# Optimization experiments

Hardware: AMD Instinct MI355X
Metric: run time of the kernel (lower is better)

## Reference

```python
import jax, jax.numpy as jnp
import numpy as np

B, L, C, O, K, KN, A = 32, 4096, 256, 256, 3, 4, 16
BN_EPS = 1e-5


def setup_inputs() -> dict:
    key = jax.random.key(0)
    ks = jax.random.split(key, 12)
    x = jax.random.normal(ks[0], (B, L, C), dtype=jnp.float32)
    # ODConv weight bank [kernel_num, out, in//groups, k], kaiming-ish scale
    weight = jax.random.normal(ks[1], (KN, O, C, K), dtype=jnp.float32) * np.sqrt(2.0 / (O * K))
    w_fc = jax.random.normal(ks[2], (A, C), dtype=jnp.float32) * np.sqrt(2.0 / A)
    bn_gamma = jnp.ones((A,), jnp.float32)
    bn_beta = jnp.zeros((A,), jnp.float32)
    bn_mean = jnp.zeros((A,), jnp.float32)
    bn_var = jnp.ones((A,), jnp.float32)
    w_ch = jax.random.normal(ks[3], (C, A), dtype=jnp.float32) * np.sqrt(2.0 / C)
    b_ch = jnp.zeros((C,), jnp.float32)
    w_fil = jax.random.normal(ks[4], (O, A), dtype=jnp.float32) * np.sqrt(2.0 / O)
    b_fil = jnp.zeros((O,), jnp.float32)
    w_sp = jax.random.normal(ks[5], (K, A), dtype=jnp.float32) * np.sqrt(2.0 / K)
    b_sp = jnp.zeros((K,), jnp.float32)
    w_ker = jax.random.normal(ks[6], (KN, A), dtype=jnp.float32) * np.sqrt(2.0 / KN)
    b_ker = jnp.zeros((KN,), jnp.float32)
    return {"x": x, "weight": weight, "w_fc": w_fc, "bn_gamma": bn_gamma,
            "bn_beta": bn_beta, "bn_mean": bn_mean, "bn_var": bn_var,
            "w_ch": w_ch, "b_ch": b_ch, "w_fil": w_fil, "b_fil": b_fil,
            "w_sp": w_sp, "b_sp": b_sp, "w_ker": w_ker, "b_ker": b_ker}


def reference(x, weight, w_fc, bn_gamma, bn_beta, bn_mean, bn_var,
              w_ch, b_ch, w_fil, b_fil, w_sp, b_sp, w_ker, b_ker):
    # x: [B, L, C] channels-last; attention head uses global-avg-pooled features
    pooled = x.mean(axis=1)                                   # [B, C]
    h = pooled @ w_fc.T                                       # [B, A] (1x1 conv, no bias)
    h = (h - bn_mean) * jax.lax.rsqrt(bn_var + BN_EPS) * bn_gamma + bn_beta
    h = jax.nn.relu(h)
    # temperature = 1.0
    ch_att = jax.nn.sigmoid(h @ w_ch.T + b_ch)                # [B, C]  channel attention
    fil_att = jax.nn.sigmoid(h @ w_fil.T + b_fil)             # [B, O]  filter attention
    sp_att = jax.nn.sigmoid(h @ w_sp.T + b_sp)                # [B, K]  spatial attention
    ker_att = jax.nn.softmax(h @ w_ker.T + b_ker, axis=1)     # [B, KN] kernel attention
    # aggregate per-sample dynamic kernel: [B, O, C, K]
    agg_w = jnp.einsum('bk,bn,noik->boik', sp_att, ker_att, weight)
    xs = x.transpose(0, 2, 1) * ch_att[:, :, None]            # [B, C, L]

    def conv1(xi, wi):  # xi: [C, L], wi: [O, C, K]
        return jax.lax.conv_general_dilated(
            xi[None], wi, window_strides=(1,), padding=[(1, 1)],
            rhs_dilation=(1,), dimension_numbers=('NCH', 'OIH', 'NCH'))[0]

    out = jax.vmap(conv1)(xs, agg_w)                          # [B, O, L]
    return out * fil_att[:, :, None]
```

## Files before the change

kernel.cpp:

```cpp
#include <hip/hip_runtime.h>
#include <hip/hip_bf16.h>
#include <stdint.h>

#define B_ 32
#define L_ 4096
#define C_ 256
#define O_ 256
#define K_ 3
#define KN_ 4
#define A_ 16

typedef unsigned short u16;
typedef __attribute__((ext_vector_type(8))) short bf16x8;
typedef __attribute__((ext_vector_type(4))) float f32x4;

static __device__ __forceinline__ u16 f2bf(float f) {
    union { float f; uint32_t u; } v; v.f = f;
    uint32_t u = v.u;
    u += 0x7fffu + ((u >> 16) & 1u);
    return (u16)(u >> 16);
}

__global__ __launch_bounds__(256) void pool_partial_k(const float* __restrict__ x,
                                                      float* __restrict__ part) {
    int bid = blockIdx.x;
    int b = bid >> 5, ch = bid & 31;
    int c = threadIdx.x;
    const float* p = x + (size_t)(b * L_ + ch * 128) * C_ + c;
    float s = 0.f;
    #pragma unroll 4
    for (int l = 0; l < 128; ++l) s += p[(size_t)l * C_];
    part[((size_t)bid << 8) + c] = s;
}

__global__ __launch_bounds__(256) void att_k(const float* __restrict__ part,
    const float* __restrict__ w_fc, const float* __restrict__ bn_g,
    const float* __restrict__ bn_b, const float* __restrict__ bn_m,
    const float* __restrict__ bn_v,
    const float* __restrict__ w_ch, const float* __restrict__ b_ch,
    const float* __restrict__ w_fil, const float* __restrict__ b_fil,
    const float* __restrict__ w_sp, const float* __restrict__ b_sp,
    const float* __restrict__ w_ker, const float* __restrict__ b_ker,
    float* __restrict__ ch_att, float* __restrict__ fil_att,
    float* __restrict__ sp_att, float* __restrict__ ker_att) {
    __shared__ float pooled[C_];
    __shared__ float h[A_];
    int b = blockIdx.x, t = threadIdx.x;
    float s = 0.f;
    for (int j = 0; j < 32; ++j) s += part[(((size_t)(b * 32 + j)) << 8) + t];
    pooled[t] = s * (1.0f / L_);
    __syncthreads();
    if (t < A_) {
        float acc = 0.f;
        for (int c = 0; c < C_; ++c) acc += pooled[c] * w_fc[t * C_ + c];
        float sc = bn_g[t] * rsqrtf(bn_v[t] + 1e-5f);
        acc = (acc - bn_m[t]) * sc + bn_b[t];
        h[t] = fmaxf(acc, 0.f);
    }
    __syncthreads();
    {
        float a1 = b_ch[t], a2 = b_fil[t];
        for (int a = 0; a < A_; ++a) { a1 += h[a] * w_ch[t * A_ + a]; a2 += h[a] * w_fil[t * A_ + a]; }
        ch_att[b * C_ + t]  = 1.f / (1.f + expf(-a1));
        fil_att[b * O_ + t] = 1.f / (1.f + expf(-a2));
    }
    if (t < K_) {
        float acc = b_sp[t];
        for (int a = 0; a < A_; ++a) acc += h[a] * w_sp[t * A_ + a];
        sp_att[b * 4 + t] = 1.f / (1.f + expf(-acc));
    }
    if (t == 0) {
        float lg[KN_], m = -1e30f;
        for (int n = 0; n < KN_; ++n) {
            float acc = b_ker[n];
            for (int a = 0; a < A_; ++a) acc += h[a] * w_ker[n * A_ + a];
            lg[n] = acc; m = fmaxf(m, acc);
        }
        float ss = 0.f;
        for (int n = 0; n < KN_; ++n) { lg[n] = expf(lg[n] - m); ss += lg[n]; }
        for (int n = 0; n < KN_; ++n) ker_att[b * 4 + n] = lg[n] / ss;
    }
}

__global__ __launch_bounds__(256) void wfrag_k(const float* __restrict__ weight,
    const float* __restrict__ ch_att, const float* __restrict__ fil_att,
    const float* __restrict__ sp_att, const float* __restrict__ ker_att,
    u16* __restrict__ wf) {
    __shared__ float wlds[64 * 97];
    int beta = blockIdx.x;
    int ob = beta & 15, ic = (beta >> 4) & 7, bg = beta >> 7;
    int t = threadIdx.x;

    const size_t blk_base = (size_t)(ob * 16) * 768 + ic * 96;
    #pragma unroll
    for (int j = 0; j < 24; ++j) {
        int ei = t + (j << 8);
        int r = ei / 96, c = ei - r * 96;
        int n = r >> 4, ol = r & 15;
        wlds[r * 97 + c] = weight[((size_t)n * 256 + ol) * 768 + blk_base + c];
    }
    __syncthreads();

    int lane = t & 63, q = t >> 6;
    int o_l = lane & 15, ig = lane >> 4;
    int i0 = ig << 3;
    int o = (ob << 4) + o_l;
    int ig0 = (ic << 5) + i0;

    float wl[4][3][8];
    #pragma unroll
    for (int n = 0; n < 4; ++n) {
        int rb = (n * 16 + o_l) * 97;
        #pragma unroll
        for (int e = 0; e < 8; ++e) {
            int cb = rb + (i0 + e) * 3;
            wl[n][0][e] = wlds[cb];
            wl[n][1][e] = wlds[cb + 1];
            wl[n][2][e] = wlds[cb + 2];
        }
    }

    #pragma unroll
    for (int bi = 0; bi < 2; ++bi) {
        int b = (bg << 3) + (q << 1) + bi;
        float ka0 = ker_att[b * 4 + 0], ka1 = ker_att[b * 4 + 1];
        float ka2 = ker_att[b * 4 + 2], ka3 = ker_att[b * 4 + 3];
        float fil = fil_att[b * O_ + o];
        float ch8[8];
        *reinterpret_cast<float4*>(ch8)     = *reinterpret_cast<const float4*>(ch_att + b * C_ + ig0);
        *reinterpret_cast<float4*>(ch8 + 4) = *reinterpret_cast<const float4*>(ch_att + b * C_ + ig0 + 4);
        #pragma unroll
        for (int tap = 0; tap < 3; ++tap) {
            float fs = fil * sp_att[b * 4 + tap];
            union { u16 h[8]; uint4 v; } pk;
            #pragma unroll
            for (int e = 0; e < 8; ++e) {
                float acc = ka0 * wl[0][tap][e] + ka1 * wl[1][tap][e]
                          + ka2 * wl[2][tap][e] + ka3 * wl[3][tap][e];
                pk.h[e] = f2bf(acc * fs * ch8[e]);
            }
            size_t idx = ((((size_t)(b * 24 + tap * 8 + ic) * 16 + ob) * 64) + lane) << 3;
            *reinterpret_cast<uint4*>(wf + idx) = pk.v;
        }
    }
}

__global__ __launch_bounds__(512, 4) void conv_k(const float* __restrict__ x,
    const u16* __restrict__ wf, float* __restrict__ out) {
    __shared__ uint4 lds4[4160];
    char* lp = (char*)lds4;
    int phys = blockIdx.x;
    int logical = ((phys & 7) << 7) + (phys >> 3);
    int b = logical >> 5, lb = logical & 31;
    int l0 = lb << 7;
    int tid = threadIdx.x;
    const size_t xbase = (size_t)b * L_ * C_;

    #pragma unroll 4
    for (int it = 0; it < 17; ++it) {
        int id = tid + (it << 9);
        if (id < 8320) {
            int r  = id >> 6;
            int i  = (id & 63) << 2;
            int lg = l0 - 1 + r;
            float4 v = make_float4(0.f, 0.f, 0.f, 0.f);
            if (lg >= 0 && lg < L_)
                v = *reinterpret_cast<const float4*>(x + xbase + (size_t)lg * C_ + i);
            ushort4 hv;
            hv.x = f2bf(v.x); hv.y = f2bf(v.y); hv.z = f2bf(v.z); hv.w = f2bf(v.w);
            int slot = (i >> 3) ^ (r & 7);
            int off = r * 512 + slot * 16 + ((i >> 2) & 1) * 8;
            *reinterpret_cast<ushort4*>(lp + off) = hv;
        }
    }
    __syncthreads();

    int w = tid >> 6, lane = tid & 63;
    int wr = w & 3, wc = w >> 2;
    int lrow = lane & 15;
    int g = lane >> 4;

    f32x4 acc[4][4] = {};

    for (int kc = 0; kc < 24; ++kc) {
        int t  = kc >> 3;
        int ic = kc & 7;
        bf16x8 af[4], bfr[4];
        const u16* wp = wf + ((((size_t)(b * 24 + kc) * 16 + wr * 4) * 64 + lane) << 3);
        #pragma unroll
        for (int m = 0; m < 4; ++m)
            af[m] = *reinterpret_cast<const bf16x8*>(wp + (m << 9));
        int slotbase = (ic << 2) + g;
        #pragma unroll
        for (int n = 0; n < 4; ++n) {
            int row = wc * 64 + n * 16 + lrow + t;
            int off = row * 512 + ((slotbase ^ (row & 7)) << 4);
            bfr[n] = *reinterpret_cast<const bf16x8*>(lp + off);
        }
        #pragma unroll
        for (int m = 0; m < 4; ++m)
            #pragma unroll
            for (int n = 0; n < 4; ++n)
                acc[m][n] = __builtin_amdgcn_mfma_f32_16x16x32_bf16(af[m], bfr[n], acc[m][n], 0, 0, 0);
    }

    __syncthreads();

    float* ep = (float*)(lp + w * 8192);
    size_t obase = (size_t)b * O_ * L_;
    int lcol = l0 + wc * 64;
    #pragma unroll
    for (int c2 = 0; c2 < 2; ++c2) {
        #pragma unroll
        for (int m2 = 0; m2 < 2; ++m2) {
            int m = c2 * 2 + m2;
            #pragma unroll
            for (int n = 0; n < 4; ++n) {
                int l_loc = n * 16 + lrow;
                int sl = (l_loc >> 2);
                #pragma unroll
                for (int j = 0; j < 4; ++j) {
                    int o_loc = m2 * 16 + g * 4 + j;
                    ep[o_loc * 64 + ((sl ^ o_loc) & 15) * 4 + (l_loc & 3)] = acc[m][n][j];
                }
            }
        }
        #pragma unroll
        for (int og = 0; og < 8; ++og) {
            int o_loc = og * 4 + g;
            int l4 = lrow;
            float4 v = *reinterpret_cast<float4*>(ep + o_loc * 64 + ((l4 ^ o_loc) & 15) * 4);
            int o = wr * 64 + c2 * 32 + o_loc;
            *reinterpret_cast<float4*>(out + obase + (size_t)o * L_ + lcol + l4 * 4) = v;
        }
        if (c2 == 0) __syncthreads();
    }
}

extern "C" void kernel_launch(void* const* d_in, const int* in_sizes, int n_in,
                              void* d_out, int out_size, void* d_ws, size_t ws_size,
                              hipStream_t stream) {
    const float* x      = (const float*)d_in[0];
    const float* weight = (const float*)d_in[1];
    const float* w_fc   = (const float*)d_in[2];
    const float* bn_g   = (const float*)d_in[3];
    const float* bn_b   = (const float*)d_in[4];
    const float* bn_m   = (const float*)d_in[5];
    const float* bn_v   = (const float*)d_in[6];
    const float* w_ch   = (const float*)d_in[7];
    const float* b_ch   = (const float*)d_in[8];
    const float* w_fil  = (const float*)d_in[9];
    const float* b_fil  = (const float*)d_in[10];
    const float* w_sp   = (const float*)d_in[11];
    const float* b_sp   = (const float*)d_in[12];
    const float* w_ker  = (const float*)d_in[13];
    const float* b_ker  = (const float*)d_in[14];
    float* out = (float*)d_out;
    char*  ws  = (char*)d_ws;

    float* part    = (float*)ws;
    float* ch_att  = (float*)(ws + (1 << 20));
    float* fil_att = ch_att + 32 * 256;
    float* sp_att  = fil_att + 32 * 256;
    float* ker_att = sp_att + 32 * 4;
    u16*   wfrag   = (u16*)(ws + (1 << 20) + 70 * 1024);

    pool_partial_k<<<1024, 256, 0, stream>>>(x, part);
    att_k<<<32, 256, 0, stream>>>(part, w_fc, bn_g, bn_b, bn_m, bn_v,
                                  w_ch, b_ch, w_fil, b_fil, w_sp, b_sp, w_ker, b_ker,
                                  ch_att, fil_att, sp_att, ker_att);
    wfrag_k<<<512, 256, 0, stream>>>(weight, ch_att, fil_att, sp_att, ker_att, wfrag);
    conv_k<<<1024, 512, 0, stream>>>(x, wfrag, out);
}
```

Baseline: 107.5 us.

## Fuse bf16 conversion of x into pooling pass and stage via direct LDS loads

New measurement: 120.4 us. 12.0% more time.

```diff
diff --git a/kernel.cpp b/kernel.cpp
--- a/kernel.cpp
+++ b/kernel.cpp
@@ -9,16 +9,56 @@
 #define K_ 3
 #define KN_ 4
 #define A_ 16
+#define LP_ 4098
 
 typedef unsigned short u16;
 typedef __attribute__((ext_vector_type(8))) short bf16x8;
 typedef __attribute__((ext_vector_type(4))) float f32x4;
+
+#define GLDS16(gp, lp_) __builtin_amdgcn_global_load_lds( \
+    (const __attribute__((address_space(1))) void*)(gp),  \
+    (__attribute__((address_space(3))) void*)(lp_), 16, 0, 0)
 
 static __device__ __forceinline__ u16 f2bf(float f) {
     union { float f; uint32_t u; } v; v.f = f;
     uint32_t u = v.u;
     u += 0x7fffu + ((u >> 16) & 1u);
     return (u16)(u >> 16);
+}
+
+__global__ __launch_bounds__(256) void poolcvt_k(const float* __restrict__ x,
+                                                 u16* __restrict__ xb,
+                                                 float* __restrict__ part) {
+    __shared__ float red[4][256];
+    int bid = blockIdx.x;
+    int b = bid >> 5, chunk = bid & 31;
+    int t = threadIdx.x;
+    int w = t >> 6, lane = t & 63;
+    int c0 = lane << 2;
+    int h = lane >> 5;
+    int grp = (lane & 31) >> 1;
+    int sub = lane & 1;
+    f32x4 s = {0.f, 0.f, 0.f, 0.f};
+    const float* xp = x + ((size_t)b * L_ + (size_t)chunk * 128) * C_ + c0;
+    u16* xbb = xb + ((size_t)b * LP_ + (size_t)chunk * 128 + 1) * 256;
+    #pragma unroll 4
+    for (int it = 0; it < 32; ++it) {
+        int rl = it * 4 + w;
+        int l = chunk * 128 + rl;
+        float4 v = *reinterpret_cast<const float4*>(xp + (size_t)rl * C_);
+        s.x += v.x; s.y += v.y; s.z += v.z; s.w += v.w;
+        ushort4 hv;
+        hv.x = f2bf(v.x); hv.y = f2bf(v.y); hv.z = f2bf(v.z); hv.w = f2bf(v.w);
+        int slot = grp ^ ((l + 1) & 7);
+        *reinterpret_cast<ushort4*>(xbb + (size_t)rl * 256 + h * 128 + slot * 8 + sub * 4) = hv;
+    }
+    *reinterpret_cast<f32x4*>(&red[w][c0]) = s;
+    __syncthreads();
+    part[((size_t)bid << 8) + t] = red[0][t] + red[1][t] + red[2][t] + red[3][t];
+    if (chunk == 0 && t < 64)
+        *reinterpret_cast<ushort4*>(xb + (size_t)b * LP_ * 256 + t * 4) = make_ushort4(0, 0, 0, 0);
+    if (chunk == 31 && t < 64)
+        *reinterpret_cast<ushort4*>(xb + ((size_t)b * LP_ + LP_ - 1) * 256 + t * 4) = make_ushort4(0, 0, 0, 0);
 }
 
 __global__ __launch_bounds__(256) void pool_partial_k(const float* __restrict__ x,
@@ -90,7 +130,6 @@
     int beta = blockIdx.x;
     int ob = beta & 15, ic = (beta >> 4) & 7, bg = beta >> 7;
     int t = threadIdx.x;
-
     const size_t blk_base = (size_t)(ob * 16) * 768 + ic * 96;
     #pragma unroll
     for (int j = 0; j < 24; ++j) {
@@ -100,13 +139,11 @@
         wlds[r * 97 + c] = weight[((size_t)n * 256 + ol) * 768 + blk_base + c];
     }
     __syncthreads();
-
     int lane = t & 63, q = t >> 6;
     int o_l = lane & 15, ig = lane >> 4;
     int i0 = ig << 3;
     int o = (ob << 4) + o_l;
     int ig0 = (ic << 5) + i0;
-
     float wl[4][3][8];
     #pragma unroll
     for (int n = 0; n < 4; ++n) {
@@ -119,7 +156,6 @@
             wl[n][2][e] = wlds[cb + 2];
         }
     }
-
     #pragma unroll
     for (int bi = 0; bi < 2; ++bi) {
         int b = (bg << 3) + (q << 1) + bi;
@@ -145,7 +181,101 @@
     }
 }
 
-__global__ __launch_bounds__(512, 4) void conv_k(const float* __restrict__ x,
+__global__ __launch_bounds__(512, 4) void conv_k(const u16* __restrict__ xb,
+    const u16* __restrict__ wf, float* __restrict__ out) {
+    __shared__ uint4 lds4[4224];
+    char* lp = (char*)lds4;
+    int phys = blockIdx.x;
+    int logical = ((phys & 7) << 7) + (phys >> 3);
+    int b = logical >> 5, lb = logical & 31;
+    int l0 = lb << 7;
+    int tid = threadIdx.x;
+    int w = tid >> 6, lane = tid & 63;
+    int wr = w & 3, wc = w >> 2;
+    int lrow = lane & 15;
+    int g = lane >> 4;
+
+    const u16* xrow = xb + ((size_t)b * LP_ + l0) * 256;
+
+    auto stage_half = [&](int h, int bufoff) {
+        const u16* gb = xrow + h * 128;
+        #pragma unroll
+        for (int j = 0; j < 4; ++j) {
+            const u16* ga = gb + (size_t)(w * 16 + j * 4 + (lane >> 4)) * 256 + (lane & 15) * 8;
+            GLDS16(ga, lp + bufoff + w * 4096 + j * 1024);
+        }
+        if (w == 0) {
+            const u16* ga = gb + (size_t)(128 + ((lane >> 4) & 1)) * 256 + (lane & 15) * 8;
+            GLDS16(ga, lp + bufoff + 32768);
+        }
+    };
+
+    f32x4 acc[4][4] = {};
+
+    auto compute_half = [&](int h, int bufoff) {
+        for (int kk = 0; kk < 12; ++kk) {
+            int tap = kk >> 2, ich = kk & 3;
+            int kc = tap * 8 + h * 4 + ich;
+            bf16x8 af[4], bfr[4];
+            const u16* wp = wf + ((((size_t)(b * 24 + kc) * 16 + wr * 4) * 64 + lane) << 3);
+            #pragma unroll
+            for (int m = 0; m < 4; ++m)
+                af[m] = *reinterpret_cast<const bf16x8*>(wp + (m << 9));
+            int slotbase = (ich << 2) + g;
+            #pragma unroll
+            for (int n = 0; n < 4; ++n) {
+                int row = wc * 64 + n * 16 + lrow + tap;
+                int off = bufoff + row * 256 + (((slotbase ^ (row & 7))) << 4);
+                bfr[n] = *reinterpret_cast<const bf16x8*>(lp + off);
+            }
+            #pragma unroll
+            for (int m = 0; m < 4; ++m)
+                #pragma unroll
+                for (int n = 0; n < 4; ++n)
+                    acc[m][n] = __builtin_amdgcn_mfma_f32_16x16x32_bf16(af[m], bfr[n], acc[m][n], 0, 0, 0);
+        }
+    };
+
+    stage_half(0, 0);
+    __syncthreads();
+    stage_half(1, 33792);
+    compute_half(0, 0);
+    __syncthreads();
+    compute_half(1, 33792);
+    __syncthreads();
+
+    float* ep = (float*)(lp + w * 8192);
+    size_t obase = (size_t)b * O_ * L_;
+    int lcol = l0 + wc * 64;
+    #pragma unroll
+    for (int c2 = 0; c2 < 2; ++c2) {
+        #pragma unroll
+        for (int m2 = 0; m2 < 2; ++m2) {
+            int m = c2 * 2 + m2;
+            #pragma unroll
+            for (int n = 0; n < 4; ++n) {
+                int l_loc = n * 16 + lrow;
+                int sl = (l_loc >> 2);
+                #pragma unroll
+                for (int j = 0; j < 4; ++j) {
+                    int o_loc = m2 * 16 + g * 4 + j;
+                    ep[o_loc * 64 + ((sl ^ o_loc) & 15) * 4 + (l_loc & 3)] = acc[m][n][j];
+                }
+            }
+        }
+        #pragma unroll
+        for (int og = 0; og < 8; ++og) {
+            int o_loc = og * 4 + g;
+            int l4 = lrow;
+            float4 v = *reinterpret_cast<float4*>(ep + o_loc * 64 + ((l4 ^ o_loc) & 15) * 4);
+            int o = wr * 64 + c2 * 32 + o_loc;
+            *reinterpret_cast<float4*>(out + obase + (size_t)o * L_ + lcol + l4 * 4) = v;
+        }
+        if (c2 == 0) __syncthreads();
+    }
+}
+
+__global__ __launch_bounds__(512, 4) void conv_fb_k(const float* __restrict__ x,
     const u16* __restrict__ wf, float* __restrict__ out) {
     __shared__ uint4 lds4[4160];
     char* lp = (char*)lds4;
@@ -155,7 +285,6 @@
     int l0 = lb << 7;
     int tid = threadIdx.x;
     const size_t xbase = (size_t)b * L_ * C_;
-
     #pragma unroll 4
     for (int it = 0; it < 17; ++it) {
         int id = tid + (it << 9);
@@ -174,14 +303,11 @@
         }
     }
     __syncthreads();
-
     int w = tid >> 6, lane = tid & 63;
     int wr = w & 3, wc = w >> 2;
     int lrow = lane & 15;
     int g = lane >> 4;
-
     f32x4 acc[4][4] = {};
-
     for (int kc = 0; kc < 24; ++kc) {
         int t  = kc >> 3;
         int ic = kc & 7;
@@ -203,9 +329,7 @@
             for (int n = 0; n < 4; ++n)
                 acc[m][n] = __builtin_amdgcn_mfma_f32_16x16x32_bf16(af[m], bfr[n], acc[m][n], 0, 0, 0);
     }
-
-    __syncthreads();
-
+    __syncthreads();
     float* ep = (float*)(lp + w * 8192);
     size_t obase = (size_t)b * O_ * L_;
     int lcol = l0 + wc * 64;
@@ -264,11 +388,22 @@
     float* sp_att  = fil_att + 32 * 256;
     float* ker_att = sp_att + 32 * 4;
     u16*   wfrag   = (u16*)(ws + (1 << 20) + 70 * 1024);
-
-    pool_partial_k<<<1024, 256, 0, stream>>>(x, part);
-    att_k<<<32, 256, 0, stream>>>(part, w_fc, bn_g, bn_b, bn_m, bn_v,
-                                  w_ch, b_ch, w_fil, b_fil, w_sp, b_sp, w_ker, b_ker,
-                                  ch_att, fil_att, sp_att, ker_att);
-    wfrag_k<<<512, 256, 0, stream>>>(weight, ch_att, fil_att, sp_att, ker_att, wfrag);
-    conv_k<<<1024, 512, 0, stream>>>(x, wfrag, out);
-}
+    u16*   xbf     = (u16*)(ws + (16u << 20));
+    const size_t need = (16u << 20) + (size_t)B_ * LP_ * 512;
+
+    if (ws_size >= need) {
+        poolcvt_k<<<1024, 256, 0, stream>>>(x, xbf, part);
+        att_k<<<32, 256, 0, stream>>>(part, w_fc, bn_g, bn_b, bn_m, bn_v,
+                                      w_ch, b_ch, w_fil, b_fil, w_sp, b_sp, w_ker, b_ker,
+                                      ch_att, fil_att, sp_att, ker_att);
+        wfrag_k<<<512, 256, 0, stream>>>(weight, ch_att, fil_att, sp_att, ker_att, wfrag);
+        conv_k<<<1024, 512, 0, stream>>>(xbf, wfrag, out);
+    } else {
+        pool_partial_k<<<1024, 256, 0, stream>>>(x, part);
+        att_k<<<32, 256, 0, stream>>>(part, w_fc, bn_g, bn_b, bn_m, bn_v,
+                                      w_ch, b_ch, w_fil, b_fil, w_sp, b_sp, w_ker, b_ker,
+                                      ch_att, fil_att, sp_att, ker_att);
+        wfrag_k<<<512, 256, 0, stream>>>(weight, ch_att, fil_att, sp_att, ker_att, wfrag);
+        conv_fb_k<<<1024, 512, 0, stream>>>(x, wfrag, out);
+    }
+}
```
